# Kernel tuning notes

Hardware: AMD Instinct MI355X
Metric: run time of the kernel (lower is better)

The kernel has to match this reference:

```python
import jax, jax.numpy as jnp
import numpy as np

N_COARSE = 12500
N_FINE = 50000
MIN_BASIS = 16  # (min(L_in, L_out) + 1) ** 2 with L_in = L_out = 3


def setup_inputs() -> dict:
    key = jax.random.key(0)
    ks = jax.random.split(key, 8)
    return {
        "last_inv": jax.random.normal(ks[0], (N_COARSE, 256), dtype=jnp.float32),
        "cur_inv": jax.random.normal(ks[1], (N_FINE, 256), dtype=jnp.float32),
        "last_equ": jax.random.normal(ks[2], (N_COARSE, 16, 256), dtype=jnp.float32),
        "cur_equ": jax.random.normal(ks[3], (N_FINE, 16, 256), dtype=jnp.float32),
        "upsampling": jax.random.randint(ks[4], (N_FINE,), 0, N_COARSE, dtype=jnp.int32),
        # Linear weights stored as [in, out] (torch weight is [out, in]; x @ W.T == x @ W_in_out)
        "W_last_equ": jax.random.normal(ks[5], (256, 256), dtype=jnp.float32) * 0.02,
        "W_cur_equ": jax.random.normal(ks[6], (256, 256), dtype=jnp.float32) * 0.02,
        "W_mlp": jax.random.normal(ks[7], (768, 512), dtype=jnp.float32) * 0.02,
    }


def reference(last_inv, cur_inv, last_equ, cur_equ, upsampling, W_last_equ, W_cur_equ, W_mlp):
    # nearest_upsample: gather coarse rows up to fine resolution
    li = jnp.take(last_inv, upsampling, axis=0)                 # [N_fine, 256]
    le = jnp.take(last_equ, upsampling, axis=0)[:, :MIN_BASIS]  # [N_fine, 16, 256]
    le = jnp.einsum('nbc,cd->nbd', le, W_last_equ)              # fc_last_equ (no bias)
    ce = jnp.einsum('nbc,cd->nbd', cur_equ[:, :MIN_BASIS], W_cur_equ)  # fc_cur_equ
    equ = (ce * le).mean(axis=1)                                # [N_fine, 256]
    com = jnp.concatenate([li, cur_inv, equ], axis=-1)          # [N_fine, 768]
    return com @ W_mlp                                          # LastUnaryBlock: Linear, no bias
```

## Files before the change

### kernel.cpp

```cpp
#include <hip/hip_runtime.h>
#include <hip/hip_bf16.h>

#define N_COARSE 12500
#define N_FINE   50000

typedef __bf16 bf16x8 __attribute__((ext_vector_type(8)));
typedef __bf16 bf16x4 __attribute__((ext_vector_type(4)));
typedef float  f32x4  __attribute__((ext_vector_type(4)));


__device__ __forceinline__ bf16x8 cvt8(f32x4 x, f32x4 y) {
    bf16x8 r;
    r[0] = (__bf16)x[0]; r[1] = (__bf16)x[1]; r[2] = (__bf16)x[2]; r[3] = (__bf16)x[3];
    r[4] = (__bf16)y[0]; r[5] = (__bf16)y[1]; r[6] = (__bf16)y[2]; r[7] = (__bf16)y[3];
    return r;
}

__device__ __forceinline__ void lds_barrier() {
    asm volatile("s_waitcnt lgkmcnt(0)" ::: "memory");
    __builtin_amdgcn_s_barrier();
}

__device__ __forceinline__ int swz(int row, int byte) { return byte ^ ((row & 7) << 4); }
__device__ __forceinline__ void st_a(__bf16* lds, int row, int cs, bf16x8 v) {
    *(bf16x8*)((char*)lds + swz(row, row * 512 + cs * 16)) = v;
}
__device__ __forceinline__ bf16x8 ld_a(const __bf16* lds, int row, int ka) {
    return *(const bf16x8*)((const char*)lds + swz(row, row * 512 + ka * 2));
}

template<int NT>
__device__ __forceinline__ void stage_f32(const float* __restrict__ A, long row0,
                                          __bf16* lds, int tid, long maxrow) {
    const int r0 = tid >> 5, cs = tid & 31;
    constexpr int RPI = NT / 32;
    #pragma unroll
    for (int i = 0; i < 64 / RPI; ++i) {
        int row = r0 + i * RPI;
        long gr = row0 + row; if (gr > maxrow) gr = maxrow;
        const float* p = A + gr * 256 + cs * 8;
        f32x4 x = *(const f32x4*)p, y = *(const f32x4*)(p + 4);
        st_a(lds, row, cs, cvt8(x, y));
    }
}

__device__ __forceinline__ void mfma_tile(const __bf16* lds, const bf16x8* __restrict__ packB,
                                          int N, int c0, int ksb,
                                          f32x4 (&acc)[4][4], int lane) {
    const int g = lane >> 4, r15 = lane & 15;
    #pragma unroll
    for (int ks = 0; ks < 8; ++ks) {
        bf16x8 a[4];
        #pragma unroll
        for (int rt = 0; rt < 4; ++rt)
            a[rt] = ld_a(lds, rt * 16 + r15, ks * 32 + g * 8);
        const size_t kb = (size_t)((ksb + ks) * 4 + g) * N;
        #pragma unroll
        for (int ct = 0; ct < 4; ++ct) {
            bf16x8 b = packB[kb + c0 + ct * 16 + r15];
            #pragma unroll
            for (int rt = 0; rt < 4; ++rt)
                acc[rt][ct] = __builtin_amdgcn_mfma_f32_16x16x32_bf16(a[rt], b, acc[rt][ct], 0, 0, 0);
        }
    }
}

__global__ __launch_bounds__(256) void k_prep(
    const float* __restrict__ W_le, const float* __restrict__ W_ce,
    const float* __restrict__ W_mlp, const float* __restrict__ last_inv,
    __bf16* __restrict__ packLE, __bf16* __restrict__ packCE,
    __bf16* __restrict__ packM, __bf16* __restrict__ li_bf)
{
    const int b = blockIdx.x, tid = threadIdx.x;
    if (b < 256) {
        int idx = b * 256 + tid, k = idx >> 8, n = idx & 255;
        packLE[(((size_t)(k >> 3) << 8) + n) * 8 + (k & 7)] = (__bf16)W_le[idx];
    } else if (b < 512) {
        int idx = (b - 256) * 256 + tid, k = idx >> 8, n = idx & 255;
        packCE[(((size_t)(k >> 3) << 8) + n) * 8 + (k & 7)] = (__bf16)W_ce[idx];
    } else if (b < 2048) {
        int idx = (b - 512) * 256 + tid, k = idx >> 9, n = idx & 511;
        packM[(((size_t)(k >> 3) << 9) + n) * 8 + (k & 7)] = (__bf16)W_mlp[idx];
    } else {
        int i = (b - 2048) * 256 + tid;
        f32x4 v = ((const f32x4*)last_inv)[i];
        bf16x4 o;
        o[0] = (__bf16)v[0]; o[1] = (__bf16)v[1]; o[2] = (__bf16)v[2]; o[3] = (__bf16)v[3];
        ((bf16x4*)li_bf)[i] = o;
    }
}

__global__ __launch_bounds__(256) void k_coarse_equ(
    const float* __restrict__ last_equ, const bf16x8* __restrict__ packW,
    __bf16* __restrict__ LEp)
{
    __shared__ __attribute__((aligned(16))) __bf16 As[64 * 256];
    const int tid = threadIdx.x, lane = tid & 63, wid = tid >> 6;
    for (int t = blockIdx.x; t < N_COARSE * 16 / 64; t += gridDim.x) {
        stage_f32<256>(last_equ, (long)t * 64, As, tid, (long)N_COARSE * 16 - 1);
        lds_barrier();
        f32x4 acc[4][4] = {};
        mfma_tile(As, packW, 256, wid * 64, 0, acc, lane);
        #pragma unroll
        for (int rt = 0; rt < 4; ++rt) {
            int coarse = t * 4 + rt;
            #pragma unroll
            for (int ct = 0; ct < 4; ++ct) {
                int cg = wid * 4 + ct;
                bf16x4 v;
                v[0] = (__bf16)acc[rt][ct][0]; v[1] = (__bf16)acc[rt][ct][1];
                v[2] = (__bf16)acc[rt][ct][2]; v[3] = (__bf16)acc[rt][ct][3];
                *(bf16x4*)(LEp + ((size_t)(coarse * 16 + cg) * 64 + lane) * 4) = v;
            }
        }
        lds_barrier();
    }
}

__global__ __launch_bounds__(256) void k_fine_equ(
    const float* __restrict__ cur_equ, const bf16x8* __restrict__ packW,
    const __bf16* __restrict__ LEp, const int* __restrict__ up,
    __bf16* __restrict__ equ)
{
    __shared__ __attribute__((aligned(16))) __bf16 As[64 * 256];
    const int tid = threadIdx.x, lane = tid & 63, wid = tid >> 6;
    for (int t = blockIdx.x; t < N_FINE / 4; t += gridDim.x) {
        const int n0 = t * 4;
        int cu[4];
        #pragma unroll
        for (int rt = 0; rt < 4; ++rt) cu[rt] = up[n0 + rt];

        stage_f32<256>(cur_equ, (long)t * 64, As, tid, (long)N_FINE * 16 - 1);
        lds_barrier();

        f32x4 acc[4][4] = {};
        mfma_tile(As, packW, 256, wid * 64, 0, acc, lane);

        bf16x4 le[4][4];
        #pragma unroll
        for (int rt = 0; rt < 4; ++rt)
            #pragma unroll
            for (int ct = 0; ct < 4; ++ct)
                le[rt][ct] = *(const bf16x4*)(LEp +
                    ((size_t)(cu[rt] * 16 + wid * 4 + ct) * 64 + lane) * 4);

        #pragma unroll
        for (int rt = 0; rt < 4; ++rt) {
            int n = n0 + rt;
            #pragma unroll
            for (int ct = 0; ct < 4; ++ct) {
                float s = acc[rt][ct][0] * (float)le[rt][ct][0]
                        + acc[rt][ct][1] * (float)le[rt][ct][1]
                        + acc[rt][ct][2] * (float)le[rt][ct][2]
                        + acc[rt][ct][3] * (float)le[rt][ct][3];
                s += __shfl_xor(s, 16, 64);
                s += __shfl_xor(s, 32, 64);
                if (lane < 16)
                    equ[(size_t)n * 256 + wid * 64 + ct * 16 + lane] =
                        (__bf16)(s * 0.0625f);
            }
        }
        lds_barrier();
    }
}

__global__ __launch_bounds__(512) void k_out(
    const __bf16* __restrict__ li_bf, const float* __restrict__ cur_inv,
    const __bf16* __restrict__ equ, const bf16x8* __restrict__ packW,
    const int* __restrict__ up, float* __restrict__ out)
{
    __shared__ __attribute__((aligned(16))) __bf16 As[64 * 256];
    const int tid = threadIdx.x, lane = tid & 63, wid = tid >> 6;
    const int row0 = blockIdx.x * 64;
    const int c0 = wid * 64;
    const int r0 = tid >> 5, cs = tid & 31;
    f32x4 acc[4][4] = {};

    #pragma unroll
    for (int i = 0; i < 4; ++i) {
        int row = r0 + i * 16;
        int gr = row0 + row; if (gr > N_FINE - 1) gr = N_FINE - 1;
        st_a(As, row, cs, *(const bf16x8*)(li_bf + (size_t)up[gr] * 256 + cs * 8));
    }
    lds_barrier();
    mfma_tile(As, packW, 512, c0, 0, acc, lane);
    lds_barrier();

    stage_f32<512>(cur_inv, row0, As, tid, N_FINE - 1);
    lds_barrier();
    mfma_tile(As, packW, 512, c0, 8, acc, lane);
    lds_barrier();

    #pragma unroll
    for (int i = 0; i < 4; ++i) {
        int row = r0 + i * 16;
        int gr = row0 + row; if (gr > N_FINE - 1) gr = N_FINE - 1;
        st_a(As, row, cs, *(const bf16x8*)(equ + (size_t)gr * 256 + cs * 8));
    }
    lds_barrier();
    mfma_tile(As, packW, 512, c0, 16, acc, lane);

    const int g = lane >> 4, r15 = lane & 15;
    #pragma unroll
    for (int rt = 0; rt < 4; ++rt)
        #pragma unroll
        for (int j = 0; j < 4; ++j) {
            int r = row0 + rt * 16 + g * 4 + j;
            if (r < N_FINE)
                #pragma unroll
                for (int ct = 0; ct < 4; ++ct)
                    out[(size_t)r * 512 + c0 + ct * 16 + r15] = acc[rt][ct][j];
        }
}

extern "C" void kernel_launch(void* const* d_in, const int* in_sizes, int n_in,
                              void* d_out, int out_size, void* d_ws, size_t ws_size,
                              hipStream_t stream) {
    const float* last_inv = (const float*)d_in[0];
    const float* cur_inv  = (const float*)d_in[1];
    const float* last_equ = (const float*)d_in[2];
    const float* cur_equ  = (const float*)d_in[3];
    const int*   up       = (const int*)d_in[4];
    const float* W_le     = (const float*)d_in[5];
    const float* W_ce     = (const float*)d_in[6];
    const float* W_mlp    = (const float*)d_in[7];
    float* out = (float*)d_out;

    char* w = (char*)d_ws;
    __bf16* LEp    = (__bf16*)w;  w += (size_t)N_COARSE * 16 * 256 * 2;
    __bf16* equ    = (__bf16*)w;  w += (size_t)N_FINE * 256 * 2;
    __bf16* li_bf  = (__bf16*)w;  w += (size_t)N_COARSE * 256 * 2;
    __bf16* packLE = (__bf16*)w;  w += (size_t)256 * 256 * 2;
    __bf16* packCE = (__bf16*)w;  w += (size_t)256 * 256 * 2;
    __bf16* packM  = (__bf16*)w;  w += (size_t)768 * 512 * 2;

    k_prep<<<2048 + 3125, 256, 0, stream>>>(
        W_le, W_ce, W_mlp, last_inv, packLE, packCE, packM, li_bf);

    k_coarse_equ<<<1280, 256, 0, stream>>>(
        last_equ, (const bf16x8*)packLE, LEp);

    k_fine_equ<<<1280, 256, 0, stream>>>(
        cur_equ, (const bf16x8*)packCE, LEp, up, equ);

    k_out<<<(N_FINE + 63) / 64, 512, 0, stream>>>(
        li_bf, cur_inv, equ, (const bf16x8*)packM, up, out);
}
```

Baseline: 522.3 us.

## Fuse coarse equivariant projection into fine kernel via direct gather of last_equ

Removes the separate coarse-level projection kernel and its bf16 intermediate buffer. Each fine tile now gathers its coarse last_equ rows directly, converts them to bf16 in LDS and runs the W_last_equ MFMA inline before the cur_equ projection. This eliminates one launch and the write and re-read of the intermediate. The cost is recomputing the coarse GEMM for every fine row, about four times the MFMA work, and gathering fp32 rows instead of bf16.

Measured after the change: 1.242 ms. 138% more time.

```diff
diff --git a/kernel.cpp b/kernel.cpp
--- a/kernel.cpp
+++ b/kernel.cpp
@@ -90,59 +90,54 @@
     }
 }
 
-__global__ __launch_bounds__(256) void k_coarse_equ(
-    const float* __restrict__ last_equ, const bf16x8* __restrict__ packW,
-    __bf16* __restrict__ LEp)
+__global__ __launch_bounds__(256) void k_fine_equ(
+    const float* __restrict__ last_equ, const float* __restrict__ cur_equ,
+    const bf16x8* __restrict__ packLE, const bf16x8* __restrict__ packCE,
+    const int* __restrict__ up, __bf16* __restrict__ equ)
 {
     __shared__ __attribute__((aligned(16))) __bf16 As[64 * 256];
     const int tid = threadIdx.x, lane = tid & 63, wid = tid >> 6;
-    for (int t = blockIdx.x; t < N_COARSE * 16 / 64; t += gridDim.x) {
-        stage_f32<256>(last_equ, (long)t * 64, As, tid, (long)N_COARSE * 16 - 1);
-        lds_barrier();
-        f32x4 acc[4][4] = {};
-        mfma_tile(As, packW, 256, wid * 64, 0, acc, lane);
-        #pragma unroll
-        for (int rt = 0; rt < 4; ++rt) {
-            int coarse = t * 4 + rt;
-            #pragma unroll
-            for (int ct = 0; ct < 4; ++ct) {
-                int cg = wid * 4 + ct;
-                bf16x4 v;
-                v[0] = (__bf16)acc[rt][ct][0]; v[1] = (__bf16)acc[rt][ct][1];
-                v[2] = (__bf16)acc[rt][ct][2]; v[3] = (__bf16)acc[rt][ct][3];
-                *(bf16x4*)(LEp + ((size_t)(coarse * 16 + cg) * 64 + lane) * 4) = v;
-            }
-        }
-        lds_barrier();
-    }
-}
-
-__global__ __launch_bounds__(256) void k_fine_equ(
-    const float* __restrict__ cur_equ, const bf16x8* __restrict__ packW,
-    const __bf16* __restrict__ LEp, const int* __restrict__ up,
-    __bf16* __restrict__ equ)
-{
-    __shared__ __attribute__((aligned(16))) __bf16 As[64 * 256];
-    const int tid = threadIdx.x, lane = tid & 63, wid = tid >> 6;
+    const int r0 = tid >> 5, cs = tid & 31;
+
     for (int t = blockIdx.x; t < N_FINE / 4; t += gridDim.x) {
         const int n0 = t * 4;
         int cu[4];
         #pragma unroll
         for (int rt = 0; rt < 4; ++rt) cu[rt] = up[n0 + rt];
 
+        #pragma unroll
+        for (int i = 0; i < 8; ++i) {
+            const long gr = (long)cu[i >> 1] * 16 + (i & 1) * 8 + r0;
+            const float* p = last_equ + gr * 256 + cs * 8;
+            f32x4 x = *(const f32x4*)p, y = *(const f32x4*)(p + 4);
+            st_a(As, i * 8 + r0, cs, cvt8(x, y));
+        }
+        lds_barrier();
+
+        f32x4 acc[4][4] = {};
+        mfma_tile(As, packLE, 256, wid * 64, 0, acc, lane);
+
+        bf16x4 le[4][4];
+        #pragma unroll
+        for (int rt = 0; rt < 4; ++rt)
+            #pragma unroll
+            for (int ct = 0; ct < 4; ++ct) {
+                le[rt][ct][0] = (__bf16)acc[rt][ct][0];
+                le[rt][ct][1] = (__bf16)acc[rt][ct][1];
+                le[rt][ct][2] = (__bf16)acc[rt][ct][2];
+                le[rt][ct][3] = (__bf16)acc[rt][ct][3];
+            }
+        lds_barrier();
+
         stage_f32<256>(cur_equ, (long)t * 64, As, tid, (long)N_FINE * 16 - 1);
         lds_barrier();
 
-        f32x4 acc[4][4] = {};
-        mfma_tile(As, packW, 256, wid * 64, 0, acc, lane);
-
-        bf16x4 le[4][4];
         #pragma unroll
         for (int rt = 0; rt < 4; ++rt)
             #pragma unroll
             for (int ct = 0; ct < 4; ++ct)
-                le[rt][ct] = *(const bf16x4*)(LEp +
-                    ((size_t)(cu[rt] * 16 + wid * 4 + ct) * 64 + lane) * 4);
+                acc[rt][ct] = f32x4{0.f, 0.f, 0.f, 0.f};
+        mfma_tile(As, packCE, 256, wid * 64, 0, acc, lane);
 
         #pragma unroll
         for (int rt = 0; rt < 4; ++rt) {
@@ -227,7 +222,6 @@
     float* out = (float*)d_out;
 
     char* w = (char*)d_ws;
-    __bf16* LEp    = (__bf16*)w;  w += (size_t)N_COARSE * 16 * 256 * 2;
     __bf16* equ    = (__bf16*)w;  w += (size_t)N_FINE * 256 * 2;
     __bf16* li_bf  = (__bf16*)w;  w += (size_t)N_COARSE * 256 * 2;
     __bf16* packLE = (__bf16*)w;  w += (size_t)256 * 256 * 2;
@@ -237,11 +231,8 @@
     k_prep<<<2048 + 3125, 256, 0, stream>>>(
         W_le, W_ce, W_mlp, last_inv, packLE, packCE, packM, li_bf);
 
-    k_coarse_equ<<<1280, 256, 0, stream>>>(
-        last_equ, (const bf16x8*)packLE, LEp);
-
     k_fine_equ<<<1280, 256, 0, stream>>>(
-        cur_equ, (const bf16x8*)packCE, LEp, up, equ);
+        last_equ, cur_equ, (const bf16x8*)packLE, (const bf16x8*)packCE, up, equ);
 
     k_out<<<(N_FINE + 63) / 64, 512, 0, stream>>>(
         li_bf, cur_inv, equ, (const bf16x8*)packM, up, out);
```

## Double-buffer fine-equ fp32 tiles via direct global-to-LDS loads

Applied to the files above, without the earlier changes.

Rewrites k_fine_equ so each block handles a contiguous range of 2-node (32-row) tiles. The next tile's fp32 rows are prefetched straight into a double-buffered LDS region with global_load_lds, using a swizzled source address, while the current tile is converted to bf16 and fed to MFMA. This overlaps the dominant cur_equ HBM stream with compute and drops the register staging pass. The grid shrinks to 512 persistent blocks and each block uses more LDS (64KB), which may cut occupancy.

Measured after the change: 516.4 us. No clear change (-1.1%).

```diff
diff --git a/kernel.cpp b/kernel.cpp
--- a/kernel.cpp
+++ b/kernel.cpp
@@ -19,6 +19,12 @@
 __device__ __forceinline__ void lds_barrier() {
     asm volatile("s_waitcnt lgkmcnt(0)" ::: "memory");
     __builtin_amdgcn_s_barrier();
+}
+
+__device__ __forceinline__ void gl_lds16(const float* g, float* l) {
+    __builtin_amdgcn_global_load_lds(
+        (const __attribute__((address_space(1))) void*)g,
+        (__attribute__((address_space(3))) void*)l, 16, 0, 0);
 }
 
 __device__ __forceinline__ int swz(int row, int byte) { return byte ^ ((row & 7) << 4); }
@@ -122,31 +128,72 @@
     const __bf16* __restrict__ LEp, const int* __restrict__ up,
     __bf16* __restrict__ equ)
 {
-    __shared__ __attribute__((aligned(16))) __bf16 As[64 * 256];
+    __shared__ __attribute__((aligned(16))) float Af[2][32 * 256];
     const int tid = threadIdx.x, lane = tid & 63, wid = tid >> 6;
-    for (int t = blockIdx.x; t < N_FINE / 4; t += gridDim.x) {
-        const int n0 = t * 4;
-        int cu[4];
-        #pragma unroll
-        for (int rt = 0; rt < 4; ++rt) cu[rt] = up[n0 + rt];
-
-        stage_f32<256>(cur_equ, (long)t * 64, As, tid, (long)N_FINE * 16 - 1);
-        lds_barrier();
-
-        f32x4 acc[4][4] = {};
-        mfma_tile(As, packW, 256, wid * 64, 0, acc, lane);
-
-        bf16x4 le[4][4];
-        #pragma unroll
-        for (int rt = 0; rt < 4; ++rt)
-            #pragma unroll
-            for (int ct = 0; ct < 4; ++ct)
-                le[rt][ct] = *(const bf16x4*)(LEp +
-                    ((size_t)(cu[rt] * 16 + wid * 4 + ct) * 64 + lane) * 4);
-
-        #pragma unroll
-        for (int rt = 0; rt < 4; ++rt) {
-            int n = n0 + rt;
+    const int g = lane >> 4, r15 = lane & 15;
+    const int NT = N_FINE / 2;
+    const int per = (NT + gridDim.x - 1) / gridDim.x;
+    const int tb = blockIdx.x * per;
+    const int te = min(tb + per, NT);
+    if (tb >= te) return;
+
+    const int lhalf = (lane & 1) << 2;
+
+    {
+        const float* rb = cur_equ + (size_t)tb * 32 * 256;
+        #pragma unroll
+        for (int i = 0; i < 8; ++i) {
+            int row = wid * 8 + i;
+            gl_lds16(rb + (size_t)row * 256 + ((((lane >> 1) ^ (row & 7)) << 3) + lhalf),
+                     &Af[tb & 1][row * 256]);
+        }
+    }
+
+    for (int t = tb; t < te; ++t) {
+        asm volatile("s_waitcnt vmcnt(0)" ::: "memory");
+        __builtin_amdgcn_s_barrier();
+
+        if (t + 1 < te) {
+            const float* rb = cur_equ + (size_t)(t + 1) * 32 * 256;
+            #pragma unroll
+            for (int i = 0; i < 8; ++i) {
+                int row = wid * 8 + i;
+                gl_lds16(rb + (size_t)row * 256 + ((((lane >> 1) ^ (row & 7)) << 3) + lhalf),
+                         &Af[(t + 1) & 1][row * 256]);
+            }
+        }
+
+        const float* B = Af[t & 1];
+        f32x4 acc[2][4] = {};
+        #pragma unroll
+        for (int ks = 0; ks < 8; ++ks) {
+            bf16x8 a[2];
+            #pragma unroll
+            for (int rt = 0; rt < 2; ++rt) {
+                int r = rt * 16 + r15;
+                const float* p = B + r * 256 + (((4 * ks + g) ^ (r & 7)) << 3);
+                a[rt] = cvt8(*(const f32x4*)p, *(const f32x4*)(p + 4));
+            }
+            const size_t kb = (size_t)(ks * 4 + g) * 256;
+            #pragma unroll
+            for (int ct = 0; ct < 4; ++ct) {
+                bf16x8 b = packW[kb + wid * 64 + ct * 16 + r15];
+                #pragma unroll
+                for (int rt = 0; rt < 2; ++rt)
+                    acc[rt][ct] = __builtin_amdgcn_mfma_f32_16x16x32_bf16(a[rt], b, acc[rt][ct], 0, 0, 0);
+            }
+        }
+
+        const int n0 = t * 2;
+        const int cu0 = up[n0], cu1 = up[n0 + 1];
+        bf16x4 le[2][4];
+        #pragma unroll
+        for (int ct = 0; ct < 4; ++ct) {
+            le[0][ct] = *(const bf16x4*)(LEp + ((size_t)(cu0 * 16 + wid * 4 + ct) * 64 + lane) * 4);
+            le[1][ct] = *(const bf16x4*)(LEp + ((size_t)(cu1 * 16 + wid * 4 + ct) * 64 + lane) * 4);
+        }
+        #pragma unroll
+        for (int rt = 0; rt < 2; ++rt) {
             #pragma unroll
             for (int ct = 0; ct < 4; ++ct) {
                 float s = acc[rt][ct][0] * (float)le[rt][ct][0]
@@ -156,11 +203,10 @@
                 s += __shfl_xor(s, 16, 64);
                 s += __shfl_xor(s, 32, 64);
                 if (lane < 16)
-                    equ[(size_t)n * 256 + wid * 64 + ct * 16 + lane] =
+                    equ[(size_t)(n0 + rt) * 256 + wid * 64 + ct * 16 + lane] =
                         (__bf16)(s * 0.0625f);
             }
         }
-        lds_barrier();
     }
 }
 
@@ -240,7 +286,7 @@
     k_coarse_equ<<<1280, 256, 0, stream>>>(
         last_equ, (const bf16x8*)packLE, LEp);
 
-    k_fine_equ<<<1280, 256, 0, stream>>>(
+    k_fine_equ<<<512, 256, 0, stream>>>(
         cur_equ, (const bf16x8*)packCE, LEp, up, equ);
 
     k_out<<<(N_FINE + 63) / 64, 512, 0, stream>>>(
```
